# Kernel tuning notes

Hardware: AMD Instinct MI355X
Metric: run time of the kernel (lower is better)

## Reference

```python
import jax, jax.numpy as jnp
import numpy as np
import math

EMBED_DIM = 768
NUM_HEADS = 12
HEAD_DIM = EMBED_DIM // NUM_HEADS
B, L = 8, 1024


def setup_inputs() -> dict:
    key = jax.random.key(0)
    ks = jax.random.split(key, 10)
    s = 1.0 / math.sqrt(EMBED_DIM)
    x = jax.random.normal(ks[0], (B, L, EMBED_DIM), dtype=jnp.float32)
    attention_mask = jnp.ones((B, L), dtype=jnp.int32)
    # torch nn.Linear weights: shape (out, in), y = x @ W.T + b
    Wq = jax.random.normal(ks[1], (EMBED_DIM, EMBED_DIM), jnp.float32) * s
    bq = jnp.zeros((EMBED_DIM,), jnp.float32)
    Wk = jax.random.normal(ks[2], (EMBED_DIM, EMBED_DIM), jnp.float32) * s
    bk = jnp.zeros((EMBED_DIM,), jnp.float32)
    Wv = jax.random.normal(ks[3], (EMBED_DIM, EMBED_DIM), jnp.float32) * s
    bv = jnp.zeros((EMBED_DIM,), jnp.float32)
    Wo = jax.random.normal(ks[4], (EMBED_DIM, EMBED_DIM), jnp.float32) * s
    bo = jnp.zeros((EMBED_DIM,), jnp.float32)
    return {"x": x, "attention_mask": attention_mask,
            "Wq": Wq, "bq": bq, "Wk": Wk, "bk": bk,
            "Wv": Wv, "bv": bv, "Wo": Wo, "bo": bo}


def reference(x, attention_mask, Wq, bq, Wk, bk, Wv, bv, Wo, bo):
    # NOTE: faithful to the original buggy forward:
    #   V = K_embed(x); scores = K @ K^T; Q unused; scale by sqrt(embed_dim);
    #   mask broadcasts over the KEY axis (masks entire query rows).
    b, l, d = x.shape
    K = x @ Wk.T + bk                                  # (B,L,D)
    Q = x @ Wq.T + bq                                  # computed but unused (as in source)
    V = K                                              # V = self.K_embed(x)
    Kh = K.reshape(b, l, NUM_HEADS, HEAD_DIM).transpose(0, 2, 1, 3)  # (B,H,L,dh)
    Vh = V.reshape(b, l, NUM_HEADS, HEAD_DIM).transpose(0, 2, 1, 3)
    scores = jnp.einsum('bhid,bhjd->bhij', Kh, Kh) / math.sqrt(EMBED_DIM)
    if attention_mask is not None:
        row_mask = attention_mask[:, None, :, None]    # (B,1,L,1) -> masks query rows
        scores = jnp.where(row_mask == 0, jnp.float32(-1e9), scores)
    attn = jax.nn.softmax(scores, axis=-1)             # dropout p=0 -> identity
    wV = jnp.einsum('bhij,bhjd->bhid', attn, Vh)       # (B,H,L,dh)
    wV = wV.transpose(0, 2, 1, 3).reshape(b, l, d)     # (B,L,D)
    out = wV @ Wo.T + bo
    return out
```

## Files before the change

### kernel.cpp

```cpp
#include <hip/hip_runtime.h>
#include <hip/hip_bf16.h>

#define NUM_B 8
#define SEQ 1024
#define DIM 768
#define NH 12
#define DH 64

typedef __attribute__((ext_vector_type(8))) short bf16x8;
typedef __attribute__((ext_vector_type(4))) float floatx4;
typedef __attribute__((ext_vector_type(4))) unsigned short ushortx4;
typedef __attribute__((ext_vector_type(8))) unsigned short ushortx8;

__device__ __forceinline__ unsigned short f2bf(float f) {
  unsigned u = __float_as_uint(f);
  u += 0x7FFFu + ((u >> 16) & 1u);
  return (unsigned short)(u >> 16);
}

#define GLOAD16(g, l) __builtin_amdgcn_global_load_lds( \
    (const __attribute__((address_space(1))) unsigned int*)(g), \
    (__attribute__((address_space(3))) unsigned int*)(l), 16, 0, 0)

__global__ __launch_bounds__(256) void convert_kernel(
    const float* __restrict__ x, const float* __restrict__ Wk,
    const float* __restrict__ Wo, unsigned short* __restrict__ xb,
    unsigned short* __restrict__ Wkb, unsigned short* __restrict__ Wob)
{
  const int NX4 = (8192 * 768) / 4;
  const int NW4 = (768 * 768) / 4;
  int i = blockIdx.x * 256 + threadIdx.x;
  const float* s; unsigned short* d; int off;
  if (i < NX4)            { s = x;  d = xb;  off = i; }
  else if (i < NX4 + NW4) { s = Wk; d = Wkb; off = i - NX4; }
  else                    { s = Wo; d = Wob; off = i - NX4 - NW4; }
  float4 v = ((const float4*)s)[off];
  ushortx4 h;
  h.x = f2bf(v.x); h.y = f2bf(v.y); h.z = f2bf(v.z); h.w = f2bf(v.w);
  ((ushortx4*)d)[off] = h;
}

__global__ __launch_bounds__(256) void proj_k_kernel(
    const unsigned short* __restrict__ xb, const unsigned short* __restrict__ Wkb,
    const float* __restrict__ bk, unsigned short* __restrict__ Kbh,
    unsigned short* __restrict__ KbhT)
{
  __shared__ __align__(16) unsigned short smem[24576];
  const int tid = threadIdx.x;
  const int lane = tid & 63;
  const int w = tid >> 6;
  const int wr = w >> 1, wc = w & 1;
  const int quad = lane >> 4, r16 = lane & 15;
  const int rs = r16 & 7;
  const int m0 = blockIdx.x * 64, n0 = blockIdx.y * 128;
  const int wbase = (tid & ~63);

  floatx4 acc[2][4] = {};

  auto stage = [&](int kt, int buf) {
    unsigned short* As = smem + buf * 12288;
    unsigned short* Bs = As + 4096;
#pragma unroll
    for (int i = 0; i < 2; ++i) {
      int c = tid + i * 256;
      int row = c >> 3, g = (c & 7) ^ (row & 7);
      GLOAD16(xb + (size_t)(m0 + row) * DIM + kt + g * 8,
              As + (size_t)(wbase + i * 256) * 8);
    }
#pragma unroll
    for (int i = 0; i < 4; ++i) {
      int c = tid + i * 256;
      int row = c >> 3, g = (c & 7) ^ (row & 7);
      GLOAD16(Wkb + (size_t)(n0 + row) * DIM + kt + g * 8,
              Bs + (size_t)(wbase + i * 256) * 8);
    }
  };

  stage(0, 0);
  int buf = 0;
  for (int it = 0; it < 12; ++it) {
    __syncthreads();
    if (it + 1 < 12) stage((it + 1) * 64, buf ^ 1);
    const unsigned short* As = smem + buf * 12288;
    const unsigned short* Bs = As + 4096;
    bf16x8 af[2][2], bfm[4][2];
#pragma unroll
    for (int mi = 0; mi < 2; ++mi)
#pragma unroll
      for (int kc = 0; kc < 2; ++kc)
        af[mi][kc] = *(const bf16x8*)&As[(wr * 32 + mi * 16 + r16) * 64 + ((kc * 4 + quad) ^ rs) * 8];
#pragma unroll
    for (int ni = 0; ni < 4; ++ni)
#pragma unroll
      for (int kc = 0; kc < 2; ++kc)
        bfm[ni][kc] = *(const bf16x8*)&Bs[(wc * 64 + ni * 16 + r16) * 64 + ((kc * 4 + quad) ^ rs) * 8];
#pragma unroll
    for (int mi = 0; mi < 2; ++mi)
#pragma unroll
      for (int ni = 0; ni < 4; ++ni) {
        acc[mi][ni] = __builtin_amdgcn_mfma_f32_16x16x32_bf16(af[mi][0], bfm[ni][0], acc[mi][ni], 0, 0, 0);
        acc[mi][ni] = __builtin_amdgcn_mfma_f32_16x16x32_bf16(af[mi][1], bfm[ni][1], acc[mi][ni], 0, 0, 0);
      }
    buf ^= 1;
  }

  __syncthreads();
  unsigned short* Ct = smem;
  const int bb = m0 >> 10, l0 = m0 & 1023;
#pragma unroll
  for (int mi = 0; mi < 2; ++mi)
#pragma unroll
    for (int ni = 0; ni < 4; ++ni) {
      int col = n0 + wc * 64 + ni * 16 + r16;
      float bias = bk[col];
      int hh = col >> 6, dd = col & 63;
      ushortx4 pk;
#pragma unroll
      for (int r = 0; r < 4; ++r) {
        int mrow = wr * 32 + mi * 16 + quad * 4 + r;
        unsigned short us = f2bf(acc[mi][ni][r] + bias);
        Kbh[((size_t)(bb * NH + hh) * SEQ + l0 + mrow) * DH + dd] = us;
        pk[r] = us;
      }
      *(ushortx4*)&Ct[(wc * 64 + ni * 16 + r16) * 72 + wr * 32 + mi * 16 + quad * 4] = pk;
    }
  __syncthreads();
#pragma unroll
  for (int i = 0; i < 4; ++i) {
    int c = tid + i * 256;
    int row = c >> 3, ch = c & 7;
    ushortx8 v = *(const ushortx8*)&Ct[row * 72 + ch * 8];
    int j = n0 + row;
    int hh = j >> 6, dd = j & 63;
    *(ushortx8*)&KbhT[((size_t)(bb * NH + hh) * DH + dd) * SEQ + l0 + ch * 8] = v;
  }
}

__global__ __launch_bounds__(512) void attn_kernel(
    const unsigned short* __restrict__ Kbh, const unsigned short* __restrict__ KbhT,
    const int* __restrict__ mask, unsigned short* __restrict__ wV)
{
  __shared__ __align__(16) unsigned short smem[25344];
  unsigned short* Ps = smem + 16384;
  float* rsum = (float*)&smem[25088];

  const int tid = threadIdx.x;
  const int lane = tid & 63;
  const int w = tid >> 6;
  const int quad = lane >> 4, r16 = lane & 15;
  const int rs = r16 & 7;
  const int Lb = blockIdx.x;
  const int qt = (Lb >> 3) & 7;
  const int bh = (Lb >> 6) * 8 + (Lb & 7);
  const int b = bh / NH, h = bh % NH;
  const unsigned short* Kb  = Kbh  + (size_t)bh * SEQ * DH;
  const unsigned short* KbT = KbhT + (size_t)bh * DH * SEQ;
  const int q0 = qt * 128;
  const int qw = w * 16;
  const int wbase = (tid & ~63);
  const float SCALE2 = 0.036084391824351615f * 1.4426950408889634f;

  bf16x8 aq[2];
#pragma unroll
  for (int kc = 0; kc < 2; ++kc)
    aq[kc] = *(const bf16x8*)(Kb + (size_t)(q0 + qw + r16) * DH + kc * 32 + quad * 8);

  const float scm = (mask[b * SEQ + q0 + qw + r16] != 0) ? SCALE2 : 0.0f;

  floatx4 accO[4] = {};
  float psum = 0.0f;

  auto stage = [&](int kt, int buf) {
    unsigned short* Ks  = smem + buf * 4096;
    unsigned short* KTs = smem + 8192 + buf * 4096;
    int row = tid >> 3, g = (tid & 7) ^ (row & 7);
    GLOAD16(Kb + (size_t)(kt + row) * DH + g * 8,
            Ks + (size_t)wbase * 8);
    GLOAD16(KbT + (size_t)row * SEQ + kt + g * 8,
            KTs + (size_t)wbase * 8);
  };

  stage(0, 0);
  int buf = 0;
  for (int it = 0; it < SEQ / 64; ++it) {
    __syncthreads();
    if (it + 1 < SEQ / 64) stage((it + 1) * 64, buf ^ 1);
    const unsigned short* Ks  = smem + buf * 4096;
    const unsigned short* KTs = smem + 8192 + buf * 4096;

    floatx4 St[4] = {};
    __builtin_amdgcn_s_setprio(1);
#pragma unroll
    for (int kt = 0; kt < 4; ++kt) {
      int rb = (kt * 16 + r16) * 64;
      bf16x8 k0 = *(const bf16x8*)&Ks[rb + ((quad) ^ rs) * 8];
      bf16x8 k1 = *(const bf16x8*)&Ks[rb + ((4 + quad) ^ rs) * 8];
      St[kt] = __builtin_amdgcn_mfma_f32_16x16x32_bf16(k0, aq[0], St[kt], 0, 0, 0);
      St[kt] = __builtin_amdgcn_mfma_f32_16x16x32_bf16(k1, aq[1], St[kt], 0, 0, 0);
    }
    __builtin_amdgcn_s_setprio(0);

    {
      int prow = (qw + r16) * 68 + quad * 4;
#pragma unroll
      for (int kt = 0; kt < 4; ++kt) {
        float p0 = __builtin_amdgcn_exp2f(St[kt][0] * scm);
        float p1 = __builtin_amdgcn_exp2f(St[kt][1] * scm);
        float p2 = __builtin_amdgcn_exp2f(St[kt][2] * scm);
        float p3 = __builtin_amdgcn_exp2f(St[kt][3] * scm);
        psum += (p0 + p1) + (p2 + p3);
        __hip_bfloat162 lo = __float22bfloat162_rn(make_float2(p0, p1));
        __hip_bfloat162 hi = __float22bfloat162_rn(make_float2(p2, p3));
        unsigned u0, u1;
        __builtin_memcpy(&u0, &lo, 4);
        __builtin_memcpy(&u1, &hi, 4);
        *(uint2*)&Ps[prow + kt * 16] = make_uint2(u0, u1);
      }
    }

    bf16x8 ap[2];
#pragma unroll
    for (int kc = 0; kc < 2; ++kc)
      ap[kc] = *(const bf16x8*)&Ps[(qw + r16) * 68 + kc * 32 + quad * 8];
    __builtin_amdgcn_s_setprio(1);
#pragma unroll
    for (int ni = 0; ni < 4; ++ni) {
      int rb = (ni * 16 + r16) * 64;
      bf16x8 v0 = *(const bf16x8*)&KTs[rb + ((quad) ^ rs) * 8];
      bf16x8 v1 = *(const bf16x8*)&KTs[rb + ((4 + quad) ^ rs) * 8];
      accO[ni] = __builtin_amdgcn_mfma_f32_16x16x32_bf16(ap[0], v0, accO[ni], 0, 0, 0);
      accO[ni] = __builtin_amdgcn_mfma_f32_16x16x32_bf16(ap[1], v1, accO[ni], 0, 0, 0);
    }
    __builtin_amdgcn_s_setprio(0);
    buf ^= 1;
  }

  {
    float s = psum;
    s += __shfl_xor(s, 16);
    s += __shfl_xor(s, 32);
    if (quad == 0) rsum[qw + r16] = s;
  }
  float rinv[4];
#pragma unroll
  for (int r = 0; r < 4; ++r)
    rinv[r] = 1.0f / rsum[qw + quad * 4 + r];

#pragma unroll
  for (int ni = 0; ni < 4; ++ni)
#pragma unroll
    for (int r = 0; r < 4; ++r) {
      int l = q0 + qw + quad * 4 + r;
      int col = h * DH + ni * 16 + r16;
      wV[(size_t)(b * SEQ + l) * DIM + col] = f2bf(accO[ni][r] * rinv[r]);
    }
}

__global__ __launch_bounds__(256) void proj_o_kernel(
    const unsigned short* __restrict__ wVb, const unsigned short* __restrict__ Wob,
    const float* __restrict__ bo, float* __restrict__ out)
{
  __shared__ __align__(16) unsigned short smem[24576];
  const int tid = threadIdx.x;
  const int lane = tid & 63;
  const int w = tid >> 6;
  const int wr = w >> 1, wc = w & 1;
  const int quad = lane >> 4, r16 = lane & 15;
  const int rs = r16 & 7;
  const int m0 = blockIdx.x * 64, n0 = blockIdx.y * 128;
  const int wbase = (tid & ~63);

  floatx4 acc[2][4] = {};

  auto stage = [&](int kt, int buf) {
    unsigned short* As = smem + buf * 12288;
    unsigned short* Bs = As + 4096;
#pragma unroll
    for (int i = 0; i < 2; ++i) {
      int c = tid + i * 256;
      int row = c >> 3, g = (c & 7) ^ (row & 7);
      GLOAD16(wVb + (size_t)(m0 + row) * DIM + kt + g * 8,
              As + (size_t)(wbase + i * 256) * 8);
    }
#pragma unroll
    for (int i = 0; i < 4; ++i) {
      int c = tid + i * 256;
      int row = c >> 3, g = (c & 7) ^ (row & 7);
      GLOAD16(Wob + (size_t)(n0 + row) * DIM + kt + g * 8,
              Bs + (size_t)(wbase + i * 256) * 8);
    }
  };

  stage(0, 0);
  int buf = 0;
  for (int it = 0; it < 12; ++it) {
    __syncthreads();
    if (it + 1 < 12) stage((it + 1) * 64, buf ^ 1);
    const unsigned short* As = smem + buf * 12288;
    const unsigned short* Bs = As + 4096;
    bf16x8 af[2][2], bfm[4][2];
#pragma unroll
    for (int mi = 0; mi < 2; ++mi)
#pragma unroll
      for (int kc = 0; kc < 2; ++kc)
        af[mi][kc] = *(const bf16x8*)&As[(wr * 32 + mi * 16 + r16) * 64 + ((kc * 4 + quad) ^ rs) * 8];
#pragma unroll
    for (int ni = 0; ni < 4; ++ni)
#pragma unroll
      for (int kc = 0; kc < 2; ++kc)
        bfm[ni][kc] = *(const bf16x8*)&Bs[(wc * 64 + ni * 16 + r16) * 64 + ((kc * 4 + quad) ^ rs) * 8];
#pragma unroll
    for (int mi = 0; mi < 2; ++mi)
#pragma unroll
      for (int ni = 0; ni < 4; ++ni) {
        acc[mi][ni] = __builtin_amdgcn_mfma_f32_16x16x32_bf16(af[mi][0], bfm[ni][0], acc[mi][ni], 0, 0, 0);
        acc[mi][ni] = __builtin_amdgcn_mfma_f32_16x16x32_bf16(af[mi][1], bfm[ni][1], acc[mi][ni], 0, 0, 0);
      }
    buf ^= 1;
  }

#pragma unroll
  for (int mi = 0; mi < 2; ++mi)
#pragma unroll
    for (int ni = 0; ni < 4; ++ni) {
      int col = n0 + wc * 64 + ni * 16 + r16;
      float bias = bo[col];
#pragma unroll
      for (int r = 0; r < 4; ++r) {
        int row = m0 + wr * 32 + mi * 16 + quad * 4 + r;
        out[(size_t)row * DIM + col] = acc[mi][ni][r] + bias;
      }
    }
}

extern "C" void kernel_launch(void* const* d_in, const int* in_sizes, int n_in,
                              void* d_out, int out_size, void* d_ws, size_t ws_size,
                              hipStream_t stream) {
  const float* x  = (const float*)d_in[0];
  const int* mask = (const int*)d_in[1];
  const float* Wk = (const float*)d_in[4];
  const float* bk = (const float*)d_in[5];
  const float* Wo = (const float*)d_in[8];
  const float* bo = (const float*)d_in[9];
  float* out = (float*)d_out;

  unsigned short* p = (unsigned short*)d_ws;
  unsigned short* xb   = p;  p += (size_t)8192 * 768;
  unsigned short* Wkb  = p;  p += (size_t)768 * 768;
  unsigned short* Wob  = p;  p += (size_t)768 * 768;
  unsigned short* Kbh  = p;  p += (size_t)NUM_B * NH * SEQ * DH;
  unsigned short* KbhT = p;  p += (size_t)NUM_B * NH * SEQ * DH;
  unsigned short* wVb  = p;

  convert_kernel<<<7296, 256, 0, stream>>>(x, Wk, Wo, xb, Wkb, Wob);
  proj_k_kernel<<<dim3(128, 6), 256, 0, stream>>>(xb, Wkb, bk, Kbh, KbhT);
  attn_kernel<<<768, 512, 0, stream>>>(Kbh, KbhT, mask, wVb);
  proj_o_kernel<<<dim3(128, 6), 256, 0, stream>>>(wVb, Wob, bo, out);
}
```

Measured before the change: 173.4 us.

## Fuse fp32-to-bf16 conversion into projection GEMM loads and prescale query

Drops the separate conversion kernel. The K and O projection GEMMs now load fp32 inputs and weights into registers, convert them to bf16, and store them to shared memory, with register-staged double buffering. This removes one launch and the write and reread of the bf16 copies. The attention kernel folds the softmax scale and mask into the query fragment, so each score no longer needs a multiply; the trade is that the query is rounded to bf16 after scaling, which can slightly change accuracy. The projections also set an occupancy hint of 3 blocks per SM, and their fp32 global loads now go through registers instead of direct-to-LDS loads.

Result: slower. 186.5 us (+7.6%).

```diff
diff --git a/kernel.cpp b/kernel.cpp
--- a/kernel.cpp
+++ b/kernel.cpp
@@ -18,30 +18,25 @@
   return (unsigned short)(u >> 16);
 }
 
+__device__ __forceinline__ ushortx8 pk8(float4 a, float4 b) {
+  __hip_bfloat162 h0 = __float22bfloat162_rn(make_float2(a.x, a.y));
+  __hip_bfloat162 h1 = __float22bfloat162_rn(make_float2(a.z, a.w));
+  __hip_bfloat162 h2 = __float22bfloat162_rn(make_float2(b.x, b.y));
+  __hip_bfloat162 h3 = __float22bfloat162_rn(make_float2(b.z, b.w));
+  unsigned u0, u1, u2, u3;
+  __builtin_memcpy(&u0, &h0, 4); __builtin_memcpy(&u1, &h1, 4);
+  __builtin_memcpy(&u2, &h2, 4); __builtin_memcpy(&u3, &h3, 4);
+  uint4 t = make_uint4(u0, u1, u2, u3);
+  ushortx8 r; __builtin_memcpy(&r, &t, 16);
+  return r;
+}
+
 #define GLOAD16(g, l) __builtin_amdgcn_global_load_lds( \
     (const __attribute__((address_space(1))) unsigned int*)(g), \
     (__attribute__((address_space(3))) unsigned int*)(l), 16, 0, 0)
 
-__global__ __launch_bounds__(256) void convert_kernel(
+__global__ __launch_bounds__(256, 3) void proj_k_kernel(
     const float* __restrict__ x, const float* __restrict__ Wk,
-    const float* __restrict__ Wo, unsigned short* __restrict__ xb,
-    unsigned short* __restrict__ Wkb, unsigned short* __restrict__ Wob)
-{
-  const int NX4 = (8192 * 768) / 4;
-  const int NW4 = (768 * 768) / 4;
-  int i = blockIdx.x * 256 + threadIdx.x;
-  const float* s; unsigned short* d; int off;
-  if (i < NX4)            { s = x;  d = xb;  off = i; }
-  else if (i < NX4 + NW4) { s = Wk; d = Wkb; off = i - NX4; }
-  else                    { s = Wo; d = Wob; off = i - NX4 - NW4; }
-  float4 v = ((const float4*)s)[off];
-  ushortx4 h;
-  h.x = f2bf(v.x); h.y = f2bf(v.y); h.z = f2bf(v.z); h.w = f2bf(v.w);
-  ((ushortx4*)d)[off] = h;
-}
-
-__global__ __launch_bounds__(256) void proj_k_kernel(
-    const unsigned short* __restrict__ xb, const unsigned short* __restrict__ Wkb,
     const float* __restrict__ bk, unsigned short* __restrict__ Kbh,
     unsigned short* __restrict__ KbhT)
 {
@@ -53,34 +48,43 @@
   const int quad = lane >> 4, r16 = lane & 15;
   const int rs = r16 & 7;
   const int m0 = blockIdx.x * 64, n0 = blockIdx.y * 128;
-  const int wbase = (tid & ~63);
 
   floatx4 acc[2][4] = {};
-
-  auto stage = [&](int kt, int buf) {
-    unsigned short* As = smem + buf * 12288;
-    unsigned short* Bs = As + 4096;
+  float4 ra[2][2], rb[4][2];
+
+  auto issue = [&](int kt) {
 #pragma unroll
     for (int i = 0; i < 2; ++i) {
       int c = tid + i * 256;
       int row = c >> 3, g = (c & 7) ^ (row & 7);
-      GLOAD16(xb + (size_t)(m0 + row) * DIM + kt + g * 8,
-              As + (size_t)(wbase + i * 256) * 8);
+      const float4* s = (const float4*)(x + (size_t)(m0 + row) * DIM + kt + g * 8);
+      ra[i][0] = s[0]; ra[i][1] = s[1];
     }
 #pragma unroll
     for (int i = 0; i < 4; ++i) {
       int c = tid + i * 256;
       int row = c >> 3, g = (c & 7) ^ (row & 7);
-      GLOAD16(Wkb + (size_t)(n0 + row) * DIM + kt + g * 8,
-              Bs + (size_t)(wbase + i * 256) * 8);
-    }
-  };
-
-  stage(0, 0);
+      const float4* s = (const float4*)(Wk + (size_t)(n0 + row) * DIM + kt + g * 8);
+      rb[i][0] = s[0]; rb[i][1] = s[1];
+    }
+  };
+  auto commit = [&](int buf) {
+    unsigned short* As = smem + buf * 12288;
+    unsigned short* Bs = As + 4096;
+#pragma unroll
+    for (int i = 0; i < 2; ++i)
+      *(ushortx8*)&As[(size_t)(tid + i * 256) * 8] = pk8(ra[i][0], ra[i][1]);
+#pragma unroll
+    for (int i = 0; i < 4; ++i)
+      *(ushortx8*)&Bs[(size_t)(tid + i * 256) * 8] = pk8(rb[i][0], rb[i][1]);
+  };
+
+  issue(0);
+  commit(0);
+  __syncthreads();
   int buf = 0;
   for (int it = 0; it < 12; ++it) {
-    __syncthreads();
-    if (it + 1 < 12) stage((it + 1) * 64, buf ^ 1);
+    if (it + 1 < 12) issue((it + 1) * 64);
     const unsigned short* As = smem + buf * 12288;
     const unsigned short* Bs = As + 4096;
     bf16x8 af[2][2], bfm[4][2];
@@ -101,10 +105,11 @@
         acc[mi][ni] = __builtin_amdgcn_mfma_f32_16x16x32_bf16(af[mi][0], bfm[ni][0], acc[mi][ni], 0, 0, 0);
         acc[mi][ni] = __builtin_amdgcn_mfma_f32_16x16x32_bf16(af[mi][1], bfm[ni][1], acc[mi][ni], 0, 0, 0);
       }
+    if (it + 1 < 12) commit(buf ^ 1);
+    __syncthreads();
     buf ^= 1;
   }
 
-  __syncthreads();
   unsigned short* Ct = smem;
   const int bb = m0 >> 10, l0 = m0 & 1023;
 #pragma unroll
@@ -160,12 +165,25 @@
   const int wbase = (tid & ~63);
   const float SCALE2 = 0.036084391824351615f * 1.4426950408889634f;
 
+  const float scm = (mask[b * SEQ + q0 + qw + r16] != 0) ? SCALE2 : 0.0f;
+
   bf16x8 aq[2];
 #pragma unroll
-  for (int kc = 0; kc < 2; ++kc)
-    aq[kc] = *(const bf16x8*)(Kb + (size_t)(q0 + qw + r16) * DH + kc * 32 + quad * 8);
-
-  const float scm = (mask[b * SEQ + q0 + qw + r16] != 0) ? SCALE2 : 0.0f;
+  for (int kc = 0; kc < 2; ++kc) {
+    bf16x8 v = *(const bf16x8*)(Kb + (size_t)(q0 + qw + r16) * DH + kc * 32 + quad * 8);
+    ushortx8 u; __builtin_memcpy(&u, &v, 16);
+    ushortx8 o;
+#pragma unroll
+    for (int j = 0; j < 8; j += 2) {
+      float f0 = __uint_as_float(((unsigned)u[j]) << 16) * scm;
+      float f1 = __uint_as_float(((unsigned)u[j + 1]) << 16) * scm;
+      __hip_bfloat162 hh = __float22bfloat162_rn(make_float2(f0, f1));
+      unsigned hu; __builtin_memcpy(&hu, &hh, 4);
+      o[j] = (unsigned short)(hu & 0xffffu);
+      o[j + 1] = (unsigned short)(hu >> 16);
+    }
+    __builtin_memcpy(&aq[kc], &o, 16);
+  }
 
   floatx4 accO[4] = {};
   float psum = 0.0f;
@@ -204,10 +222,10 @@
       int prow = (qw + r16) * 68 + quad * 4;
 #pragma unroll
       for (int kt = 0; kt < 4; ++kt) {
-        float p0 = __builtin_amdgcn_exp2f(St[kt][0] * scm);
-        float p1 = __builtin_amdgcn_exp2f(St[kt][1] * scm);
-        float p2 = __builtin_amdgcn_exp2f(St[kt][2] * scm);
-        float p3 = __builtin_amdgcn_exp2f(St[kt][3] * scm);
+        float p0 = __builtin_amdgcn_exp2f(St[kt][0]);
+        float p1 = __builtin_amdgcn_exp2f(St[kt][1]);
+        float p2 = __builtin_amdgcn_exp2f(St[kt][2]);
+        float p3 = __builtin_amdgcn_exp2f(St[kt][3]);
         psum += (p0 + p1) + (p2 + p3);
         __hip_bfloat162 lo = __float22bfloat162_rn(make_float2(p0, p1));
         __hip_bfloat162 hi = __float22bfloat162_rn(make_float2(p2, p3));
@@ -256,8 +274,8 @@
     }
 }
 
-__global__ __launch_bounds__(256) void proj_o_kernel(
-    const unsigned short* __restrict__ wVb, const unsigned short* __restrict__ Wob,
+__global__ __launch_bounds__(256, 3) void proj_o_kernel(
+    const unsigned short* __restrict__ wVb, const float* __restrict__ Wo,
     const float* __restrict__ bo, float* __restrict__ out)
 {
   __shared__ __align__(16) unsigned short smem[24576];
@@ -271,10 +289,10 @@
   const int wbase = (tid & ~63);
 
   floatx4 acc[2][4] = {};
-
-  auto stage = [&](int kt, int buf) {
+  float4 rb[4][2];
+
+  auto stageA = [&](int kt, int buf) {
     unsigned short* As = smem + buf * 12288;
-    unsigned short* Bs = As + 4096;
 #pragma unroll
     for (int i = 0; i < 2; ++i) {
       int c = tid + i * 256;
@@ -282,20 +300,30 @@
       GLOAD16(wVb + (size_t)(m0 + row) * DIM + kt + g * 8,
               As + (size_t)(wbase + i * 256) * 8);
     }
+  };
+  auto issueB = [&](int kt) {
 #pragma unroll
     for (int i = 0; i < 4; ++i) {
       int c = tid + i * 256;
       int row = c >> 3, g = (c & 7) ^ (row & 7);
-      GLOAD16(Wob + (size_t)(n0 + row) * DIM + kt + g * 8,
-              Bs + (size_t)(wbase + i * 256) * 8);
-    }
-  };
-
-  stage(0, 0);
+      const float4* s = (const float4*)(Wo + (size_t)(n0 + row) * DIM + kt + g * 8);
+      rb[i][0] = s[0]; rb[i][1] = s[1];
+    }
+  };
+  auto commitB = [&](int buf) {
+    unsigned short* Bs = smem + buf * 12288 + 4096;
+#pragma unroll
+    for (int i = 0; i < 4; ++i)
+      *(ushortx8*)&Bs[(size_t)(tid + i * 256) * 8] = pk8(rb[i][0], rb[i][1]);
+  };
+
+  stageA(0, 0);
+  issueB(0);
+  commitB(0);
+  __syncthreads();
   int buf = 0;
   for (int it = 0; it < 12; ++it) {
-    __syncthreads();
-    if (it + 1 < 12) stage((it + 1) * 64, buf ^ 1);
+    if (it + 1 < 12) { stageA((it + 1) * 64, buf ^ 1); issueB((it + 1) * 64); }
     const unsigned short* As = smem + buf * 12288;
     const unsigned short* Bs = As + 4096;
     bf16x8 af[2][2], bfm[4][2];
@@ -316,6 +344,8 @@
         acc[mi][ni] = __builtin_amdgcn_mfma_f32_16x16x32_bf16(af[mi][0], bfm[ni][0], acc[mi][ni], 0, 0, 0);
         acc[mi][ni] = __builtin_amdgcn_mfma_f32_16x16x32_bf16(af[mi][1], bfm[ni][1], acc[mi][ni], 0, 0, 0);
       }
+    if (it + 1 < 12) commitB(buf ^ 1);
+    __syncthreads();
     buf ^= 1;
   }
 
@@ -345,15 +375,11 @@
   float* out = (float*)d_out;
 
   unsigned short* p = (unsigned short*)d_ws;
-  unsigned short* xb   = p;  p += (size_t)8192 * 768;
-  unsigned short* Wkb  = p;  p += (size_t)768 * 768;
-  unsigned short* Wob  = p;  p += (size_t)768 * 768;
   unsigned short* Kbh  = p;  p += (size_t)NUM_B * NH * SEQ * DH;
   unsigned short* KbhT = p;  p += (size_t)NUM_B * NH * SEQ * DH;
   unsigned short* wVb  = p;
 
-  convert_kernel<<<7296, 256, 0, stream>>>(x, Wk, Wo, xb, Wkb, Wob);
-  proj_k_kernel<<<dim3(128, 6), 256, 0, stream>>>(xb, Wkb, bk, Kbh, KbhT);
+  proj_k_kernel<<<dim3(128, 6), 256, 0, stream>>>(x, Wk, bk, Kbh, KbhT);
   attn_kernel<<<768, 512, 0, stream>>>(Kbh, KbhT, mask, wVb);
-  proj_o_kernel<<<dim3(128, 6), 256, 0, stream>>>(wVb, Wob, bo, out);
-}
+  proj_o_kernel<<<dim3(128, 6), 256, 0, stream>>>(wVb, Wo, bo, out);
+}
```

## Read K tiles directly from global and fold softmax scale into query operand

Applied to the files above, without the earlier changes.

Stops staging the row-major K tile in LDS and has each wave load its K MFMA operands straight from global memory (relying on cache), which halves shared memory use and removes one async LDS copy per iteration. The softmax scale and mask factor are pre-multiplied into the bf16 query fragment, so the per-element multiply before exp2 goes away. The cost is uncoalesced, latency-exposed global loads inside the inner loop, plus extra bf16 rounding of the scaled query values.

New measurement: 220.6 us. 1.27x slower.

```diff
diff --git a/kernel.cpp b/kernel.cpp
--- a/kernel.cpp
+++ b/kernel.cpp
@@ -140,9 +140,9 @@
     const unsigned short* __restrict__ Kbh, const unsigned short* __restrict__ KbhT,
     const int* __restrict__ mask, unsigned short* __restrict__ wV)
 {
-  __shared__ __align__(16) unsigned short smem[25344];
-  unsigned short* Ps = smem + 16384;
-  float* rsum = (float*)&smem[25088];
+  __shared__ __align__(16) unsigned short smem[17152];
+  unsigned short* Ps = smem + 8192;
+  float* rsum = (float*)&smem[16896];
 
   const int tid = threadIdx.x;
   const int lane = tid & 63;
@@ -160,22 +160,32 @@
   const int wbase = (tid & ~63);
   const float SCALE2 = 0.036084391824351615f * 1.4426950408889634f;
 
+  const float scm = (mask[b * SEQ + q0 + qw + r16] != 0) ? SCALE2 : 0.0f;
+
   bf16x8 aq[2];
 #pragma unroll
-  for (int kc = 0; kc < 2; ++kc)
-    aq[kc] = *(const bf16x8*)(Kb + (size_t)(q0 + qw + r16) * DH + kc * 32 + quad * 8);
-
-  const float scm = (mask[b * SEQ + q0 + qw + r16] != 0) ? SCALE2 : 0.0f;
+  for (int kc = 0; kc < 2; ++kc) {
+    bf16x8 v = *(const bf16x8*)(Kb + (size_t)(q0 + qw + r16) * DH + kc * 32 + quad * 8);
+    ushortx8 u; __builtin_memcpy(&u, &v, 16);
+    ushortx8 o;
+#pragma unroll
+    for (int j = 0; j < 8; j += 2) {
+      float f0 = __uint_as_float(((unsigned)u[j]) << 16) * scm;
+      float f1 = __uint_as_float(((unsigned)u[j + 1]) << 16) * scm;
+      __hip_bfloat162 hh = __float22bfloat162_rn(make_float2(f0, f1));
+      unsigned hu; __builtin_memcpy(&hu, &hh, 4);
+      o[j] = (unsigned short)(hu & 0xffffu);
+      o[j + 1] = (unsigned short)(hu >> 16);
+    }
+    __builtin_memcpy(&aq[kc], &o, 16);
+  }
 
   floatx4 accO[4] = {};
   float psum = 0.0f;
 
   auto stage = [&](int kt, int buf) {
-    unsigned short* Ks  = smem + buf * 4096;
-    unsigned short* KTs = smem + 8192 + buf * 4096;
+    unsigned short* KTs = smem + buf * 4096;
     int row = tid >> 3, g = (tid & 7) ^ (row & 7);
-    GLOAD16(Kb + (size_t)(kt + row) * DH + g * 8,
-            Ks + (size_t)wbase * 8);
     GLOAD16(KbT + (size_t)row * SEQ + kt + g * 8,
             KTs + (size_t)wbase * 8);
   };
@@ -185,16 +195,16 @@
   for (int it = 0; it < SEQ / 64; ++it) {
     __syncthreads();
     if (it + 1 < SEQ / 64) stage((it + 1) * 64, buf ^ 1);
-    const unsigned short* Ks  = smem + buf * 4096;
-    const unsigned short* KTs = smem + 8192 + buf * 4096;
+    const unsigned short* KTs = smem + buf * 4096;
+    const unsigned short* Kit = Kb + (size_t)it * 64 * DH;
 
     floatx4 St[4] = {};
     __builtin_amdgcn_s_setprio(1);
 #pragma unroll
     for (int kt = 0; kt < 4; ++kt) {
-      int rb = (kt * 16 + r16) * 64;
-      bf16x8 k0 = *(const bf16x8*)&Ks[rb + ((quad) ^ rs) * 8];
-      bf16x8 k1 = *(const bf16x8*)&Ks[rb + ((4 + quad) ^ rs) * 8];
+      const unsigned short* krow = Kit + (size_t)(kt * 16 + r16) * DH;
+      bf16x8 k0 = *(const bf16x8*)(krow + quad * 8);
+      bf16x8 k1 = *(const bf16x8*)(krow + 32 + quad * 8);
       St[kt] = __builtin_amdgcn_mfma_f32_16x16x32_bf16(k0, aq[0], St[kt], 0, 0, 0);
       St[kt] = __builtin_amdgcn_mfma_f32_16x16x32_bf16(k1, aq[1], St[kt], 0, 0, 0);
     }
@@ -204,10 +214,10 @@
       int prow = (qw + r16) * 68 + quad * 4;
 #pragma unroll
       for (int kt = 0; kt < 4; ++kt) {
-        float p0 = __builtin_amdgcn_exp2f(St[kt][0] * scm);
-        float p1 = __builtin_amdgcn_exp2f(St[kt][1] * scm);
-        float p2 = __builtin_amdgcn_exp2f(St[kt][2] * scm);
-        float p3 = __builtin_amdgcn_exp2f(St[kt][3] * scm);
+        float p0 = __builtin_amdgcn_exp2f(St[kt][0]);
+        float p1 = __builtin_amdgcn_exp2f(St[kt][1]);
+        float p2 = __builtin_amdgcn_exp2f(St[kt][2]);
+        float p3 = __builtin_amdgcn_exp2f(St[kt][3]);
         psum += (p0 + p1) + (p2 + p3);
         __hip_bfloat162 lo = __float22bfloat162_rn(make_float2(p0, p1));
         __hip_bfloat162 hi = __float22bfloat162_rn(make_float2(p2, p3));
```
